# Performance work log

Hardware: AMD Instinct MI355X
Metric: run time of the kernel (lower is better)

## Reference

```python
import jax, jax.numpy as jnp
import numpy as np

N = 50000   # num nodes
E = 600000  # num edges per signed adjacency
D = 128     # feature dim
K = 10      # num_diff_layers
C = 0.15    # restart probability


def setup_inputs() -> dict:
    key = jax.random.key(0)
    ks = jax.random.split(key, 8)
    rows_p = jax.random.randint(ks[0], (E,), 0, N, dtype=jnp.int32)
    cols_p = jax.random.randint(ks[1], (E,), 0, N, dtype=jnp.int32)
    vals_p = jax.random.uniform(ks[2], (E,), dtype=jnp.float32)
    rows_m = jax.random.randint(ks[3], (E,), 0, N, dtype=jnp.int32)
    cols_m = jax.random.randint(ks[4], (E,), 0, N, dtype=jnp.int32)
    vals_m = jax.random.uniform(ks[5], (E,), dtype=jnp.float32)
    X = jax.random.normal(ks[6], (N, D), dtype=jnp.float32)
    # torch code draws old_M ~ Uniform(-1, 1) at forward time; we expose it as input
    M0 = jax.random.uniform(ks[7], (N, D), dtype=jnp.float32, minval=-1.0, maxval=1.0)
    return {"rows_p": rows_p, "cols_p": cols_p, "vals_p": vals_p,
            "rows_m": rows_m, "cols_m": cols_m, "vals_m": vals_m,
            "X": X, "M0": M0}


def _spmm(rows, cols, vals, dense):
    # COO sparse [N,N] @ dense [N,D]: gather columns, scale, scatter-add to rows
    return jax.ops.segment_sum(vals[:, None] * dense[cols], rows,
                               num_segments=dense.shape[0])


def reference(rows_p, cols_p, vals_p, rows_m, cols_m, vals_m, X, M0):
    tilda_X = C * X  # restart term
    P, M = X, M0
    for _ in range(K):
        new_P = _spmm(rows_p, cols_p, vals_p, P) + _spmm(rows_m, cols_m, vals_m, M) + tilda_X
        new_M = _spmm(rows_m, cols_m, vals_m, P) + _spmm(rows_p, cols_p, vals_p, M)
        P, M = new_P, new_M
    return (P, M)
```

## Files before the change

kernel.cpp:

```cpp
#include <hip/hip_runtime.h>
#include <math.h>


#define TB 256

__device__ __forceinline__ unsigned pack_bf16(float a, float b) {
    unsigned ua = __float_as_uint(a), ub = __float_as_uint(b);
    ua += 0x7fffu + ((ua >> 16) & 1u);
    ub += 0x7fffu + ((ub >> 16) & 1u);
    return (ua >> 16) | (ub & 0xffff0000u);
}

__device__ __forceinline__ float2 unpack_bf16(unsigned w) {
    float2 r;
    r.x = __uint_as_float(w << 16);
    r.y = __uint_as_float(w & 0xffff0000u);
    return r;
}

__global__ void zero_int_kernel(int* __restrict__ p, int n) {
    int i = blockIdx.x * blockDim.x + threadIdx.x;
    if (i < n) p[i] = 0;
}

__global__ void bucket_count_kernel(const int* __restrict__ rows_p,
                                    const int* __restrict__ rows_m,
                                    int E, int* __restrict__ bcnt) {
    __shared__ int h[128];
    for (int i = threadIdx.x; i < 128; i += TB) h[i] = 0;
    __syncthreads();
    int total = 2 * E;
    for (int e = blockIdx.x * TB + threadIdx.x; e < total; e += gridDim.x * TB) {
        int r = (e < E) ? rows_p[e] : rows_m[e - E];
        atomicAdd(&h[r >> 9], 1);
    }
    __syncthreads();
    for (int i = threadIdx.x; i < 128; i += TB)
        if (h[i]) atomicAdd(&bcnt[i], h[i]);
}

__global__ void bucket_scan_kernel(const int* __restrict__ bcnt,
                                   int* __restrict__ boff, int* __restrict__ bcur) {
    int l = threadIdx.x;
    int v0 = bcnt[l], v1 = bcnt[l + 64];
    int i0 = v0, i1 = v1;
#pragma unroll
    for (int o = 1; o < 64; o <<= 1) { int y = __shfl_up(i0, o); if (l >= o) i0 += y; }
#pragma unroll
    for (int o = 1; o < 64; o <<= 1) { int y = __shfl_up(i1, o); if (l >= o) i1 += y; }
    int t0 = __shfl(i0, 63);
    int e0 = i0 - v0;
    int e1 = i1 - v1 + t0;
    boff[l] = e0;      boff[l + 64] = e1;
    bcur[l] = e0;      bcur[l + 64] = e1;
    if (l == 63) boff[128] = i1 + t0;
}

__global__ __launch_bounds__(TB) void partition_kernel(
    const int* __restrict__ rows_p, const int* __restrict__ cols_p,
    const float* __restrict__ vals_p,
    const int* __restrict__ rows_m, const int* __restrict__ cols_m,
    const float* __restrict__ vals_m, int E,
    int* __restrict__ bcur_g, uint2* __restrict__ stage) {
    __shared__ unsigned keys[2048];
    __shared__ float    vals[2048];
    __shared__ unsigned skeys[2048];
    __shared__ float    svals[2048];
    __shared__ int h[128], boff[128], bcur[128], bbase[128];
    int tile0 = blockIdx.x * 2048;
    int cnt = min(2048, 2 * E - tile0);

    for (int i = threadIdx.x; i < cnt; i += TB) {
        int e = tile0 + i; int r, c; float v;
        if (e < E) { r = rows_p[e]; c = cols_p[e]; v = vals_p[e]; }
        else       { r = rows_m[e - E]; c = cols_m[e - E]; v = -vals_m[e - E]; }
        keys[i] = ((unsigned)r << 16) | (unsigned)c;
        vals[i] = v;
    }
    for (int i = threadIdx.x; i < 128; i += TB) { h[i] = 0; bcur[i] = 0; }
    __syncthreads();
    for (int i = threadIdx.x; i < cnt; i += TB) atomicAdd(&h[keys[i] >> 25], 1);
    __syncthreads();
    if (threadIdx.x < 64) {
        int l = threadIdx.x;
        int v0 = h[l], v1 = h[l + 64], i0 = v0, i1 = v1;
#pragma unroll
        for (int o = 1; o < 64; o <<= 1) { int y = __shfl_up(i0, o); if (l >= o) i0 += y; }
#pragma unroll
        for (int o = 1; o < 64; o <<= 1) { int y = __shfl_up(i1, o); if (l >= o) i1 += y; }
        int t0 = __shfl(i0, 63);
        boff[l] = i0 - v0;
        boff[l + 64] = i1 - v1 + t0;
    }
    __syncthreads();
    for (int i = threadIdx.x; i < cnt; i += TB) {
        unsigned k = keys[i]; int b = k >> 25;
        int p = boff[b] + atomicAdd(&bcur[b], 1);
        skeys[p] = k; svals[p] = vals[i];
    }
    __syncthreads();
    if (threadIdx.x < 128) {
        int c_ = h[threadIdx.x];
        if (c_) bbase[threadIdx.x] = atomicAdd(&bcur_g[threadIdx.x], c_);
    }
    __syncthreads();
    for (int i = threadIdx.x; i < cnt; i += TB) {
        unsigned k = skeys[i]; int b = k >> 25;
        stage[bbase[b] + (i - boff[b])] = make_uint2(k, __float_as_uint(svals[i]));
    }
}

__global__ __launch_bounds__(TB) void csr_finalize_kernel(
    const uint2* __restrict__ stage, const int* __restrict__ boff_g,
    int NBv, int N, int E2, int* __restrict__ off, int2* __restrict__ edge) {
    __shared__ int rc[512], ro[512], rcur[512];
    int b = blockIdx.x;
    int row0 = b << 9;
    int s0 = boff_g[b], s1 = boff_g[b + 1];
    for (int i = threadIdx.x; i < 512; i += TB) { rc[i] = 0; rcur[i] = 0; }
    __syncthreads();
    for (int i = s0 + threadIdx.x; i < s1; i += TB)
        atomicAdd(&rc[(stage[i].x >> 16) - row0], 1);
    __syncthreads();
    if (threadIdx.x < 64) {
        int l = threadIdx.x;
        int s = 0, loc[8];
#pragma unroll
        for (int j = 0; j < 8; ++j) { loc[j] = s; s += rc[l * 8 + j]; }
        int incl = s;
#pragma unroll
        for (int o = 1; o < 64; o <<= 1) { int y = __shfl_up(incl, o); if (l >= o) incl += y; }
        int base = incl - s;
#pragma unroll
        for (int j = 0; j < 8; ++j) ro[l * 8 + j] = base + loc[j];
    }
    __syncthreads();
    for (int i = threadIdx.x; i < 512; i += TB) {
        int r = row0 + i;
        if (r < N) off[r] = s0 + ro[i];
    }
    if (b == NBv - 1 && threadIdx.x == 0) off[N] = E2;
    for (int i = s0 + threadIdx.x; i < s1; i += TB) {
        uint2 rec = stage[i];
        int lr = (int)(rec.x >> 16) - row0;
        int p = s0 + ro[lr] + atomicAdd(&rcur[lr], 1);
        edge[p] = make_int2((int)(rec.x & 0xffffu), (int)rec.y);
    }
}

__global__ void init_kernel(const float* __restrict__ X, const float* __restrict__ M0,
                            uint2* __restrict__ SD, uint2* __restrict__ tXb, int n32) {
    int i = blockIdx.x * blockDim.x + threadIdx.x;
    if (i < n32) {
        int r = i >> 5, q = i & 31;
        float4 x = ((const float4*)X)[(size_t)r * 32 + q];
        float4 m = ((const float4*)M0)[(size_t)r * 32 + q];
        SD[(size_t)r * 64 + q]      = make_uint2(pack_bf16(x.x + m.x, x.y + m.y),
                                                 pack_bf16(x.z + m.z, x.w + m.w));
        SD[(size_t)r * 64 + 32 + q] = make_uint2(pack_bf16(x.x - m.x, x.y - m.y),
                                                 pack_bf16(x.z - m.z, x.w - m.w));
        tXb[(size_t)r * 32 + q]     = make_uint2(pack_bf16(0.15f * x.x, 0.15f * x.y),
                                                 pack_bf16(0.15f * x.z, 0.15f * x.w));
    }
}

__global__ __launch_bounds__(TB) void layer_kernel(
    const int* __restrict__ off, const int2* __restrict__ edge,
    const uint2* __restrict__ In, uint2* __restrict__ Out,
    const uint2* __restrict__ tXb,
    float* __restrict__ Pout, float* __restrict__ Mout, int last, int N) {
    int row = blockIdx.x * 4 + (threadIdx.x >> 6);
    if (row >= N) return;
    int lane = threadIdx.x & 63;
    int sel = lane >> 5;
    int q = lane & 31;

    uint2 t = tXb[(size_t)row * 32 + q];
    float2 t0 = unpack_bf16(t.x), t1 = unpack_bf16(t.y);
    float a0 = t0.x, a1 = t0.y, a2 = t1.x, a3 = t1.y;

    int bg = off[row], e = off[row + 1];
    int j = bg;
    for (; j + 8 <= e; j += 8) {
        int2 e0 = edge[j],     e1 = edge[j + 1], e2 = edge[j + 2], e3 = edge[j + 3];
        int2 e4 = edge[j + 4], e5 = edge[j + 5], e6 = edge[j + 6], e7 = edge[j + 7];
        uint2 w0 = In[(size_t)e0.x * 64 + lane];
        uint2 w1 = In[(size_t)e1.x * 64 + lane];
        uint2 w2 = In[(size_t)e2.x * 64 + lane];
        uint2 w3 = In[(size_t)e3.x * 64 + lane];
        uint2 w4 = In[(size_t)e4.x * 64 + lane];
        uint2 w5 = In[(size_t)e5.x * 64 + lane];
        uint2 w6 = In[(size_t)e6.x * 64 + lane];
        uint2 w7 = In[(size_t)e7.x * 64 + lane];
        float v0 = __int_as_float(e0.y), v1 = __int_as_float(e1.y);
        float v2 = __int_as_float(e2.y), v3 = __int_as_float(e3.y);
        float v4 = __int_as_float(e4.y), v5 = __int_as_float(e5.y);
        float v6 = __int_as_float(e6.y), v7 = __int_as_float(e7.y);
        if (!sel) {
            v0 = fabsf(v0); v1 = fabsf(v1); v2 = fabsf(v2); v3 = fabsf(v3);
            v4 = fabsf(v4); v5 = fabsf(v5); v6 = fabsf(v6); v7 = fabsf(v7);
        }
        float2 g0a = unpack_bf16(w0.x), g0b = unpack_bf16(w0.y);
        float2 g1a = unpack_bf16(w1.x), g1b = unpack_bf16(w1.y);
        float2 g2a = unpack_bf16(w2.x), g2b = unpack_bf16(w2.y);
        float2 g3a = unpack_bf16(w3.x), g3b = unpack_bf16(w3.y);
        float2 g4a = unpack_bf16(w4.x), g4b = unpack_bf16(w4.y);
        float2 g5a = unpack_bf16(w5.x), g5b = unpack_bf16(w5.y);
        float2 g6a = unpack_bf16(w6.x), g6b = unpack_bf16(w6.y);
        float2 g7a = unpack_bf16(w7.x), g7b = unpack_bf16(w7.y);
        a0 += v0 * g0a.x + v1 * g1a.x + v2 * g2a.x + v3 * g3a.x
            + v4 * g4a.x + v5 * g5a.x + v6 * g6a.x + v7 * g7a.x;
        a1 += v0 * g0a.y + v1 * g1a.y + v2 * g2a.y + v3 * g3a.y
            + v4 * g4a.y + v5 * g5a.y + v6 * g6a.y + v7 * g7a.y;
        a2 += v0 * g0b.x + v1 * g1b.x + v2 * g2b.x + v3 * g3b.x
            + v4 * g4b.x + v5 * g5b.x + v6 * g6b.x + v7 * g7b.x;
        a3 += v0 * g0b.y + v1 * g1b.y + v2 * g2b.y + v3 * g3b.y
            + v4 * g4b.y + v5 * g5b.y + v6 * g6b.y + v7 * g7b.y;
    }
    for (; j < e; ++j) {
        int2 ed = edge[j];
        uint2 w = In[(size_t)ed.x * 64 + lane];
        float v = __int_as_float(ed.y);
        if (!sel) v = fabsf(v);
        float2 ga = unpack_bf16(w.x), gb = unpack_bf16(w.y);
        a0 += v * ga.x; a1 += v * ga.y; a2 += v * gb.x; a3 += v * gb.y;
    }

    if (!last) {
        Out[(size_t)row * 64 + lane] = make_uint2(pack_bf16(a0, a1), pack_bf16(a2, a3));
    } else {
        float b0 = __shfl_xor(a0, 32), b1 = __shfl_xor(a1, 32);
        float b2 = __shfl_xor(a2, 32), b3 = __shfl_xor(a3, 32);
        if (sel == 0) {
            ((float4*)Pout)[(size_t)row * 32 + q] =
                make_float4(0.5f * (a0 + b0), 0.5f * (a1 + b1),
                            0.5f * (a2 + b2), 0.5f * (a3 + b3));
        } else {
            ((float4*)Mout)[(size_t)row * 32 + q] =
                make_float4(0.5f * (b0 - a0), 0.5f * (b1 - a1),
                            0.5f * (b2 - a2), 0.5f * (b3 - a3));
        }
    }
}

extern "C" void kernel_launch(void* const* d_in, const int* in_sizes, int n_in,
                              void* d_out, int out_size, void* d_ws, size_t ws_size,
                              hipStream_t stream) {
    const int*   rows_p = (const int*)d_in[0];
    const int*   cols_p = (const int*)d_in[1];
    const float* vals_p = (const float*)d_in[2];
    const int*   rows_m = (const int*)d_in[3];
    const int*   cols_m = (const int*)d_in[4];
    const float* vals_m = (const float*)d_in[5];
    const float* X      = (const float*)d_in[6];
    const float* M0     = (const float*)d_in[7];

    const int E = in_sizes[0];
    const int D = 128;
    const int N = in_sizes[6] / D;
    const int K = 10;
    const int E2 = 2 * E;
    const size_t ND = (size_t)N * D;
    const int N32 = N * 32;
    const int NBv = (N + 511) >> 9;

    float* outP = (float*)d_out;
    float* outM = outP + ND;

    char* ws = (char*)d_ws;
    size_t o = 0;
    auto alloc = [&](size_t b) -> void* {
        void* p = ws + o;
        o += (b + 255) & ~(size_t)255;
        return p;
    };
    uint2* SDA  = (uint2*)alloc((size_t)N * 64 * 8);
    uint2* SDB  = (uint2*)alloc((size_t)N * 64 * 8);
    uint2* tXb  = (uint2*)alloc((size_t)N * 32 * 8);
    int*   off  = (int*)alloc((size_t)(N + 1) * sizeof(int));
    int2*  edge = (int2*)alloc((size_t)E2 * sizeof(int2));
    int*   bcnt = (int*)alloc(128 * sizeof(int));
    int*   boff = (int*)alloc(129 * sizeof(int));
    int*   bcur = (int*)alloc(128 * sizeof(int));
    uint2* stage = SDB;

    int gN32 = (N32 + TB - 1) / TB;
    int gTiles = (E2 + 2047) / 2048;

    zero_int_kernel<<<1, 128, 0, stream>>>(bcnt, 128);
    bucket_count_kernel<<<512, TB, 0, stream>>>(rows_p, rows_m, E, bcnt);
    bucket_scan_kernel<<<1, 64, 0, stream>>>(bcnt, boff, bcur);
    partition_kernel<<<gTiles, TB, 0, stream>>>(rows_p, cols_p, vals_p,
                                                rows_m, cols_m, vals_m, E,
                                                bcur, stage);
    csr_finalize_kernel<<<NBv, TB, 0, stream>>>(stage, boff, NBv, N, E2, off, edge);

    init_kernel<<<gN32, TB, 0, stream>>>(X, M0, SDA, tXb, N32);

    int gL = (N + 3) / 4;
    uint2 *Si = SDA, *So = SDB;
    for (int k = 0; k < K; ++k) {
        int last = (k == K - 1);
        layer_kernel<<<gL, TB, 0, stream>>>(off, edge, Si, So, tXb,
                                            outP, outM, last, N);
        uint2* t = Si; Si = So; So = t;
    }
}
```

Baseline: 1.006 ms.

## Bucket CSR edges by column block per row and use nontemporal output stores

The CSR finalize pass now counts edges per (row, column-block) pair, with 16 blocks of 4096 columns, and scans those counts across the whole thread block. Edges within each row therefore end up roughly sorted by column, which should give the SpMM gathers better cache locality. The bf16 intermediate output stores are also switched to nontemporal stores so they do not displace gather data from cache. The cost is a larger shared-memory array and a more involved scan in the preprocessing kernel.

```diff
diff --git a/kernel.cpp b/kernel.cpp
--- a/kernel.cpp
+++ b/kernel.cpp
@@ -113,37 +113,54 @@
 __global__ __launch_bounds__(TB) void csr_finalize_kernel(
     const uint2* __restrict__ stage, const int* __restrict__ boff_g,
     int NBv, int N, int E2, int* __restrict__ off, int2* __restrict__ edge) {
-    __shared__ int rc[512], ro[512], rcur[512];
+    __shared__ int rc[8192];
+    __shared__ int tsum[256];
+    __shared__ int wtot[4];
     int b = blockIdx.x;
     int row0 = b << 9;
     int s0 = boff_g[b], s1 = boff_g[b + 1];
-    for (int i = threadIdx.x; i < 512; i += TB) { rc[i] = 0; rcur[i] = 0; }
-    __syncthreads();
-    for (int i = s0 + threadIdx.x; i < s1; i += TB)
-        atomicAdd(&rc[(stage[i].x >> 16) - row0], 1);
-    __syncthreads();
-    if (threadIdx.x < 64) {
-        int l = threadIdx.x;
-        int s = 0, loc[8];
-#pragma unroll
-        for (int j = 0; j < 8; ++j) { loc[j] = s; s += rc[l * 8 + j]; }
-        int incl = s;
-#pragma unroll
-        for (int o = 1; o < 64; o <<= 1) { int y = __shfl_up(incl, o); if (l >= o) incl += y; }
-        int base = incl - s;
-#pragma unroll
-        for (int j = 0; j < 8; ++j) ro[l * 8 + j] = base + loc[j];
-    }
-    __syncthreads();
-    for (int i = threadIdx.x; i < 512; i += TB) {
+    int t = threadIdx.x;
+
+    for (int i = t; i < 8192; i += TB) rc[i] = 0;
+    __syncthreads();
+    for (int i = s0 + t; i < s1; i += TB) {
+        unsigned k = stage[i].x;
+        int lr = (int)(k >> 16) - row0;
+        int cb = (int)(k & 0xffffu) >> 12;
+        atomicAdd(&rc[lr * 16 + cb], 1);
+    }
+    __syncthreads();
+    int base_i = t * 32;
+    int s = 0;
+#pragma unroll
+    for (int j = 0; j < 32; ++j) { int v = rc[base_i + j]; rc[base_i + j] = s; s += v; }
+    tsum[t] = s;
+    __syncthreads();
+    {
+        int lane = t & 63, wid = t >> 6;
+        int x = tsum[t], incl = x;
+#pragma unroll
+        for (int o = 1; o < 64; o <<= 1) { int y = __shfl_up(incl, o); if (lane >= o) incl += y; }
+        if (lane == 63) wtot[wid] = incl;
+        __syncthreads();
+        int wbase = 0;
+        for (int w = 0; w < wid; ++w) wbase += wtot[w];
+        int ebase = wbase + incl - x;
+#pragma unroll
+        for (int j = 0; j < 32; ++j) rc[base_i + j] += ebase;
+    }
+    __syncthreads();
+    for (int i = t; i < 512; i += TB) {
         int r = row0 + i;
-        if (r < N) off[r] = s0 + ro[i];
-    }
-    if (b == NBv - 1 && threadIdx.x == 0) off[N] = E2;
-    for (int i = s0 + threadIdx.x; i < s1; i += TB) {
+        if (r < N) off[r] = s0 + rc[i * 16];
+    }
+    if (b == NBv - 1 && t == 0) off[N] = E2;
+    __syncthreads();
+    for (int i = s0 + t; i < s1; i += TB) {
         uint2 rec = stage[i];
         int lr = (int)(rec.x >> 16) - row0;
-        int p = s0 + ro[lr] + atomicAdd(&rcur[lr], 1);
+        int cb = (int)(rec.x & 0xffffu) >> 12;
+        int p = s0 + atomicAdd(&rc[lr * 16 + cb], 1);
         edge[p] = make_int2((int)(rec.x & 0xffffu), (int)rec.y);
     }
 }
@@ -227,7 +244,10 @@
     }
 
     if (!last) {
-        Out[(size_t)row * 64 + lane] = make_uint2(pack_bf16(a0, a1), pack_bf16(a2, a3));
+        unsigned long long rec = (unsigned long long)pack_bf16(a0, a1)
+                               | ((unsigned long long)pack_bf16(a2, a3) << 32);
+        __builtin_nontemporal_store(rec,
+            (unsigned long long*)&Out[(size_t)row * 64 + lane]);
     } else {
         float b0 = __shfl_xor(a0, 32), b1 = __shfl_xor(a1, 32);
         float b2 = __shfl_xor(a2, 32), b3 = __shfl_xor(a3, 32);
```

New measurement: 1.010 ms. About the same (+0.4%).
